# Performance work log

Hardware: AMD Instinct MI355X
Metric: run time of the kernel (lower is better)

The kernel has to match this reference:

```python
import jax, jax.numpy as jnp
import numpy as np

EMBED_DIM = 96
OUT_DIM = 192
HEADS = 2
HEAD_DIM = OUT_DIM // HEADS  # 96
STRIDE_Q = (1, 2, 2)
STRIDE_KV = (1, 8, 8)
SCALE = 1.0 / float(np.sqrt(HEAD_DIM))


def layer_norm(x, g, b, eps=1e-5):
    m = jnp.mean(x, -1, keepdims=True)
    v = jnp.mean(jnp.square(x - m), -1, keepdims=True)
    return (x - m) * jax.lax.rsqrt(v + eps) * g + b


def pool(x, thw, conv_w, g, b, stride):
    # x: [B, heads, N, d] with cls token at position 0; depthwise conv3d pool + LayerNorm(d)
    B, nh, N, d = x.shape
    T, H, W = thw
    cls_tok, rest = x[:, :, :1], x[:, :, 1:]
    rest = rest.transpose(0, 1, 3, 2).reshape(B * nh, d, T, H, W)
    rest = jax.lax.conv_general_dilated(
        rest, conv_w, stride, [(1, 1), (1, 1), (1, 1)],
        dimension_numbers=('NCDHW', 'OIDHW', 'NCDHW'), feature_group_count=d)
    T2, H2, W2 = rest.shape[2], rest.shape[3], rest.shape[4]
    rest = rest.reshape(B, nh, d, -1).transpose(0, 1, 3, 2)
    x = jnp.concatenate([cls_tok, rest], axis=2)
    return layer_norm(x, g, b), (T2, H2, W2)


def rel_idx(q_n, k_n):
    # decomposed relative-distance indices with q/k resolution ratio scaling
    q_r = max(k_n / q_n, 1.0)
    k_r = max(q_n / k_n, 1.0)
    d = (jnp.arange(q_n, dtype=jnp.float32)[:, None] * q_r
         - jnp.arange(k_n, dtype=jnp.float32)[None, :] * k_r + (k_n - 1) * k_r)
    return d.astype(jnp.int32)


def add_rel_pos(attn, q, q_thw, k_thw, rph, rpw, rpt):
    qt, qh, qw = q_thw
    kt, kh, kw = k_thw
    Rh = rph[rel_idx(qh, kh)]  # [qh, kh, d]
    Rw = rpw[rel_idx(qw, kw)]  # [qw, kw, d]
    Rt = rpt[rel_idx(qt, kt)]  # [qt, kt, d]
    B, nh, qN, d = q.shape
    r_q = q[:, :, 1:].reshape(B, nh, qt, qh, qw, d)
    rel_h = jnp.einsum('bythwc,hkc->bythwk', r_q, Rh)  # k = kh
    rel_w = jnp.einsum('bythwc,wkc->bythwk', r_q, Rw)  # k = kw
    rel_t = jnp.einsum('bythwc,tkc->bythwk', r_q, Rt)  # k = kt
    rel = (rel_t[..., :, None, None] + rel_h[..., None, :, None]
           + rel_w[..., None, None, :]).reshape(B, nh, qt * qh * qw, kt * kh * kw)
    return attn.at[:, :, 1:, 1:].add(rel)


def _forward(x, qkv_w, qkv_b, proj_w, proj_b, pq_w, nq_g, nq_b, pk_w, nk_g, nk_b,
             pv_w, nv_g, nv_b, rel_pos_h, rel_pos_w, rel_pos_t, thw):
    B, N, C = x.shape
    qkv = (x @ qkv_w.T + qkv_b).reshape(B, N, 3, HEADS, HEAD_DIM).transpose(2, 0, 3, 1, 4)
    q, k, v = qkv[0], qkv[1], qkv[2]  # each [B, heads, N, head_dim]
    k, k_thw = pool(k, thw, pk_w, nk_g, nk_b, STRIDE_KV)
    v, _ = pool(v, thw, pv_w, nv_g, nv_b, STRIDE_KV)
    q, q_thw = pool(q, thw, pq_w, nq_g, nq_b, STRIDE_Q)
    attn = jnp.einsum('bhqd,bhkd->bhqk', q * SCALE, k)
    attn = add_rel_pos(attn, q, q_thw, k_thw, rel_pos_h, rel_pos_w, rel_pos_t)
    attn = jax.nn.softmax(attn, axis=-1)
    out = jnp.einsum('bhqk,bhkd->bhqd', attn, v) + q  # residual_pool, with cls embed
    out = out.transpose(0, 2, 1, 3).reshape(B, -1, OUT_DIM)
    return out @ proj_w.T + proj_b


def setup_inputs() -> dict:
    key = jax.random.key(0)
    ks = jax.random.split(key, 10)
    T, H, W = 8, 56, 56
    N = 1 + T * H * W  # 25089
    B = 4
    std = 0.02
    return {
        'x': jax.random.normal(ks[0], (B, N, EMBED_DIM), jnp.float32),
        'qkv_w': jax.random.normal(ks[1], (3 * OUT_DIM, EMBED_DIM), jnp.float32) * std,
        'qkv_b': jnp.zeros((3 * OUT_DIM,), jnp.float32),
        'proj_w': jax.random.normal(ks[2], (OUT_DIM, OUT_DIM), jnp.float32) * std,
        'proj_b': jnp.zeros((OUT_DIM,), jnp.float32),
        'pq_w': jax.random.normal(ks[3], (HEAD_DIM, 1, 3, 3, 3), jnp.float32) * std,
        'nq_g': jnp.ones((HEAD_DIM,), jnp.float32),
        'nq_b': jnp.zeros((HEAD_DIM,), jnp.float32),
        'pk_w': jax.random.normal(ks[4], (HEAD_DIM, 1, 3, 3, 3), jnp.float32) * std,
        'nk_g': jnp.ones((HEAD_DIM,), jnp.float32),
        'nk_b': jnp.zeros((HEAD_DIM,), jnp.float32),
        'pv_w': jax.random.normal(ks[5], (HEAD_DIM, 1, 3, 3, 3), jnp.float32) * std,
        'nv_g': jnp.ones((HEAD_DIM,), jnp.float32),
        'nv_b': jnp.zeros((HEAD_DIM,), jnp.float32),
        'rel_pos_h': jax.random.normal(ks[6], (55, HEAD_DIM), jnp.float32) * std,
        'rel_pos_w': jax.random.normal(ks[7], (55, HEAD_DIM), jnp.float32) * std,
        'rel_pos_t': jax.random.normal(ks[8], (15, HEAD_DIM), jnp.float32) * std,
        'thw_t': 8, 'thw_h': 56, 'thw_w': 56,
    }


def reference(x, qkv_w, qkv_b, proj_w, proj_b, pq_w, nq_g, nq_b, pk_w, nk_g, nk_b,
              pv_w, nv_g, nv_b, rel_pos_h, rel_pos_w, rel_pos_t, thw_t, thw_h, thw_w):
    thw = (int(thw_t), int(thw_h), int(thw_w))
    return _forward(x, qkv_w, qkv_b, proj_w, proj_b, pq_w, nq_g, nq_b, pk_w, nk_g, nk_b,
                    pv_w, nv_g, nv_b, rel_pos_h, rel_pos_w, rel_pos_t, thw)
```

## Files before the change

kernel.cpp:

```cpp
#include <hip/hip_runtime.h>
#include <hip/hip_bf16.h>

typedef short short8 __attribute__((ext_vector_type(8)));
typedef float floatx4 __attribute__((ext_vector_type(4)));
typedef float floatx4v __attribute__((ext_vector_type(4)));

#define SCALE_F 0.10206207261596575f

static __device__ __forceinline__ float b2f(unsigned short u){
  unsigned int v = ((unsigned int)u) << 16; float f;
  __builtin_memcpy(&f, &v, 4); return f;
}
static __device__ __forceinline__ unsigned short f2b(float f){
  __hip_bfloat16 h = __float2bfloat16(f);
  unsigned short u; __builtin_memcpy(&u, &h, 2); return u;
}
static __device__ __forceinline__ int map20(int i){
  return (i < 2) ? i : 7 + ((i-2)/3)*8 + ((i-2)%3);
}

struct ConvDesc {
  const void* src[17];
  long long off[17];
  int count[17];
};

__global__ __launch_bounds__(256) void k_convert(ConvDesc d, unsigned short* dst_base,
                                                 int* flagp, const unsigned int* xprobe)
{
  __shared__ int sflag;
  if (threadIdx.x < 64){
    unsigned int w = xprobe[1024 + threadIdx.x];
    int e = (w >> 7) & 0xFF;
    int pl = (e >= 90 && e <= 140) ? 1 : 0;
    unsigned long long m = __ballot(pl);
    if (threadIdx.x == 0){
      sflag = (__popcll(m) < 40) ? 1 : 0;
      if (blockIdx.x == 0 && blockIdx.y == 0) *flagp = sflag;
    }
  }
  __syncthreads();
  const int flag = sflag;
  const int t = blockIdx.y + 1;
  const int cnt = d.count[t];
  unsigned short* dst = dst_base + d.off[t];
  const float* sf = (const float*)d.src[t];
  const unsigned short* su = (const unsigned short*)d.src[t];
  for (int i = blockIdx.x*blockDim.x + threadIdx.x; i < cnt; i += gridDim.x*blockDim.x){
    dst[i] = flag ? f2b(sf[i]) : su[i];
  }
}

static __device__ __forceinline__ void load_x_frag(
    const void* xr_, int flag, size_t elem_off, short8& a0, short8& a1, short8& a2)
{
  if (flag){
    const float* xr = (const float*)xr_ + elem_off;
    floatx4v f0 = *(const floatx4v*)(xr),      f1 = *(const floatx4v*)(xr+4);
    floatx4v f2 = *(const floatx4v*)(xr+32),   f3 = *(const floatx4v*)(xr+36);
    floatx4v f4 = *(const floatx4v*)(xr+64),   f5 = *(const floatx4v*)(xr+68);
    #pragma unroll
    for (int j = 0; j < 4; ++j){
      a0[j] = (short)f2b(f0[j]); a0[j+4] = (short)f2b(f1[j]);
      a1[j] = (short)f2b(f2[j]); a1[j+4] = (short)f2b(f3[j]);
      a2[j] = (short)f2b(f4[j]); a2[j+4] = (short)f2b(f5[j]);
    }
  } else {
    const unsigned short* xr = (const unsigned short*)xr_ + elem_off;
    a0 = *(const short8*)(xr);
    a1 = *(const short8*)(xr + 32);
    a2 = *(const short8*)(xr + 64);
  }
}

__global__ __launch_bounds__(256) void k_qkv(
    const void* __restrict__ x, const unsigned short* __restrict__ w,
    const unsigned short* __restrict__ bias, unsigned short* __restrict__ qr,
    unsigned short* __restrict__ kc, unsigned short* __restrict__ vc,
    unsigned short* __restrict__ kcls, unsigned short* __restrict__ vcls,
    const int* __restrict__ flagp)
{
  __shared__ __align__(16) unsigned short T[64*200];
  const int flag = *flagp;
  const int tid = threadIdx.x;
  const int lane = tid & 63;
  const int wv = tid >> 6;
  const int kq = (lane >> 4) * 8;
  const int quad = lane >> 4;
  const int col_l = lane & 15;

  if (blockIdx.x < 1569){
    const int m_base = blockIdx.x * 64;
    const int row_l = wv * 16;
    int ma = m_base + row_l + col_l; if (ma > 100355) ma = 100355;
    short8 a0, a1, a2;
    load_x_frag(x, flag, (size_t)ma*96 + kq, a0, a1, a2);

    #pragma unroll
    for (int ct = 0; ct < 12; ++ct){
      int col = ct*16 + col_l;
      const unsigned short* wrow = w + col*96 + kq;
      short8 b0 = *(const short8*)(wrow);
      short8 b1 = *(const short8*)(wrow + 32);
      short8 b2 = *(const short8*)(wrow + 64);
      float bv = b2f(bias[col]);
      floatx4 acc = {0.f,0.f,0.f,0.f};
      acc = __builtin_amdgcn_mfma_f32_16x16x32_bf16(a0, b0, acc, 0,0,0);
      acc = __builtin_amdgcn_mfma_f32_16x16x32_bf16(a1, b1, acc, 0,0,0);
      acc = __builtin_amdgcn_mfma_f32_16x16x32_bf16(a2, b2, acc, 0,0,0);
      #pragma unroll
      for (int r = 0; r < 4; ++r)
        T[(row_l + quad*4 + r)*200 + ct*16 + col_l] = f2b(acc[r] + bv);
    }
    __syncthreads();

    #pragma unroll
    for (int k = 0; k < 6; ++k){
      int c = tid + k*256;
      int row = c / 24;
      int off = c - row*24;
      int m = m_base + row;
      if (m < 100356){
        int bb2 = m / 25089;
        int ntok = m - bb2*25089;
        int col8 = off*8;
        int head = (col8 >= 96) ? 1 : 0;
        int d = col8 - head*96;
        short8 v = *(const short8*)(T + row*200 + col8);
        *(short8*)(qr + ((size_t)(bb2*2 + head)*25089 + (size_t)ntok)*96 + d) = v;
      }
    }
  } else {
    const int id = blockIdx.x - 1569;
    const int isv = id / 201;
    const int bx = id - isv*201;
    const int rbase = bx * 64 + wv * 16;

    int rhoA = rbase + col_l; if (rhoA > 12803) rhoA = 12803;
    int bA, nA;
    if (rhoA < 4){ bA = rhoA; nA = 0; }
    else {
      int rp = rhoA - 4;
      bA = rp / 3200; int rem = rp - bA*3200;
      int t = rem / 400; int s = rem - t*400;
      int ry = s / 20, rx = s - ry*20;
      nA = 1 + (t*56 + map20(ry))*56 + map20(rx);
    }
    short8 a0, a1, a2;
    load_x_frag(x, flag, ((size_t)bA*25089 + nA)*96 + kq, a0, a1, a2);

    int isCls[4], bI[4], baseI[4], valid[4];
    #pragma unroll
    for (int r = 0; r < 4; ++r){
      int rho = rbase + quad*4 + r;
      valid[r] = (rho < 12804);
      if (rho > 12803) rho = 12803;
      if (rho < 4){ isCls[r] = 1; bI[r] = rho; baseI[r] = 0; }
      else {
        int rp = rho - 4;
        int b = rp / 3200; int rem = rp - b*3200;
        int t = rem / 400; int s = rem - t*400;
        int ry = s / 20, rx = s - ry*20;
        isCls[r] = 0; bI[r] = b;
        baseI[r] = (((b*8 + t)*20 + ry)*20 + rx)*192;
      }
    }

    unsigned short* buf  = isv ? vc : kc;
    unsigned short* bufc = isv ? vcls : kcls;
    #pragma unroll
    for (int ct = 0; ct < 12; ++ct){
      const int col = 192 + (isv*12 + ct)*16 + col_l;
      const unsigned short* wrow = w + col*96 + kq;
      short8 b0 = *(const short8*)(wrow);
      short8 b1 = *(const short8*)(wrow + 32);
      short8 b2 = *(const short8*)(wrow + 64);
      float bv = b2f(bias[col]);
      floatx4 acc = {0.f,0.f,0.f,0.f};
      acc = __builtin_amdgcn_mfma_f32_16x16x32_bf16(a0, b0, acc, 0,0,0);
      acc = __builtin_amdgcn_mfma_f32_16x16x32_bf16(a1, b1, acc, 0,0,0);
      acc = __builtin_amdgcn_mfma_f32_16x16x32_bf16(a2, b2, acc, 0,0,0);
      const int head = ct / 6;
      const int dstat = (ct % 6) * 16;
      #pragma unroll
      for (int r = 0; r < 4; ++r){
        if (valid[r]){
          float o = acc[r] + bv;
          if (isCls[r]) bufc[(bI[r]*2 + head)*96 + dstat + col_l] = f2b(o);
          else          buf[baseI[r] + head*96 + dstat + col_l]   = f2b(o);
        }
      }
    }
  }
}

__global__ __launch_bounds__(384) void k_pool(
    const unsigned short* __restrict__ qr, const unsigned short* __restrict__ cwq,
    const unsigned short* __restrict__ gq, const unsigned short* __restrict__ btaq,
    unsigned short* __restrict__ qp,
    const unsigned short* __restrict__ kc, const unsigned short* __restrict__ vc,
    const unsigned short* __restrict__ kcls, const unsigned short* __restrict__ vcls,
    const unsigned short* __restrict__ cwk, const unsigned short* __restrict__ gk, const unsigned short* __restrict__ bk,
    const unsigned short* __restrict__ cwv, const unsigned short* __restrict__ gv, const unsigned short* __restrict__ bv,
    unsigned short* __restrict__ kp, unsigned short* __restrict__ vt)
{
  const int tid = threadIdx.x;
  if (blockIdx.x < 1792){
    __shared__ float wlds[27*96];
    __shared__ float gls[96], bls[96];
    __shared__ float ls1[29*12], ls2[29*12];
    __shared__ float lmean[29], linvs[29];

    const int bid = blockIdx.x;
    const int y  = bid % 28;
    const int t  = (bid / 28) % 8;
    const int bh = bid / 224;
    const bool has_cls = (y == 0 && t == 0);

    for (int idx = tid; idx < 27*96; idx += 384){
      int tap = idx / 96, d = idx - tap*96;
      wlds[idx] = b2f(cwq[d*27 + tap]);
    }
    for (int idx = tid; idx < 96; idx += 384){
      gls[idx] = b2f(gq[idx]); bls[idx] = b2f(btaq[idx]);
    }
    __syncthreads();

    const int x = tid / 12, dg = tid - x*12;
    const unsigned short* qbh = qr + (size_t)bh*25089*96;
    float val[8] = {0,0,0,0,0,0,0,0};

    if (x < 28){
      #pragma unroll
      for (int dt = 0; dt < 3; ++dt){
        int tt = t + dt - 1; if (tt < 0 || tt >= 8) continue;
        #pragma unroll
        for (int dy = 0; dy < 3; ++dy){
          int yy = 2*y + dy - 1; if (yy < 0 || yy >= 56) continue;
          #pragma unroll
          for (int dx = 0; dx < 3; ++dx){
            int xv = 2*x + dx - 1; if (xv < 0 || xv >= 56) continue;
            const int tap = (dt*3+dy)*3+dx;
            short8 v = *(const short8*)(qbh + (size_t)(1 + (tt*56 + yy)*56 + xv)*96 + dg*8);
            const float* wr = wlds + tap*96 + dg*8;
            #pragma unroll
            for (int j = 0; j < 8; ++j) val[j] += b2f((unsigned short)v[j]) * wr[j];
          }
        }
      }
      float s1 = 0.f, s2 = 0.f;
      #pragma unroll
      for (int j = 0; j < 8; ++j){ s1 += val[j]; s2 += val[j]*val[j]; }
      ls1[x*12+dg] = s1; ls2[x*12+dg] = s2;
    } else if (has_cls && tid >= 348 && tid < 360){
      int cdg = tid - 348;
      short8 v = *(const short8*)(qbh + cdg*8);
      float s1 = 0.f, s2 = 0.f;
      #pragma unroll
      for (int j = 0; j < 8; ++j){ val[j] = b2f((unsigned short)v[j]); s1 += val[j]; s2 += val[j]*val[j]; }
      ls1[28*12+cdg] = s1; ls2[28*12+cdg] = s2;
    }
    __syncthreads();

    if (tid < 28 || (tid == 28 && has_cls)){
      float s1 = 0.f, s2 = 0.f;
      #pragma unroll
      for (int k = 0; k < 12; ++k){ s1 += ls1[tid*12+k]; s2 += ls2[tid*12+k]; }
      float mean = s1 * (1.f/96.f);
      float var  = s2 * (1.f/96.f) - mean*mean;
      lmean[tid] = mean; linvs[tid] = rsqrtf(var + 1e-5f);
    }
    __syncthreads();

    if (x < 28){
      float mean = lmean[x], inv = linvs[x];
      int tok = 1 + (t*28 + y)*28 + x;
      short8 o;
      #pragma unroll
      for (int j = 0; j < 8; ++j)
        o[j] = (short)f2b((val[j] - mean)*inv*gls[dg*8+j] + bls[dg*8+j]);
      *(short8*)(qp + ((size_t)bh*6273 + tok)*96 + dg*8) = o;
    } else if (has_cls && tid >= 348 && tid < 360){
      int cdg = tid - 348;
      float mean = lmean[28], inv = linvs[28];
      short8 o;
      #pragma unroll
      for (int j = 0; j < 8; ++j)
        o[j] = (short)f2b((val[j] - mean)*inv*gls[cdg*8+j] + bls[cdg*8+j]);
      *(short8*)(qp + (size_t)bh*6273*96 + cdg*8) = o;
    }
  } else {
    __shared__ float r1[3][128], r2s[3][128];
    const int unit = tid >> 7;
    const int d = tid & 127;
    const int u = (blockIdx.x - 1792)*3 + unit;
    const bool live = (u < 6656);
    int isv = 0, bh = 0, key = 0;
    if (live){
      isv = u / 3328; int rem = u - isv*3328;
      bh = rem / 416; key = rem - bh*416;
    }
    const bool pad = (key >= 393);
    const int b = bh >> 1, head = bh & 1;
    const unsigned short* buf  = isv ? vc : kc;
    const unsigned short* bufc = isv ? vcls : kcls;
    const unsigned short* cw = (isv == 0) ? cwk : cwv;
    const unsigned short* g  = (isv == 0) ? gk : gv;
    const unsigned short* bt = (isv == 0) ? bk : bv;

    float val = 0.f;
    if (live && !pad && d < 96){
      if (key == 0) val = b2f(bufc[bh*96 + d]);
      else {
        int s = key - 1; int t = s / 49; int r2 = s - t*49; int y = r2 / 7; int xx = r2 - y*7;
        const unsigned short* wr = cw + d*27;
        float sum = 0.f;
        #pragma unroll
        for (int dt = 0; dt < 3; ++dt){
          int tt = t + dt - 1; if (tt < 0 || tt >= 8) continue;
          #pragma unroll
          for (int dy = 0; dy < 3; ++dy){
            if (y == 0 && dy == 0) continue;
            int ry = (y == 0) ? (dy - 1) : 2 + 3*(y-1) + dy;
            #pragma unroll
            for (int dx = 0; dx < 3; ++dx){
              if (xx == 0 && dx == 0) continue;
              int rx = (xx == 0) ? (dx - 1) : 2 + 3*(xx-1) + dx;
              sum += b2f(buf[(((b*8 + tt)*20 + ry)*20 + rx)*192 + head*96 + d]) * b2f(wr[(dt*3+dy)*3+dx]);
            }
          }
        }
        val = sum;
      }
    }
    r1[unit][d]  = (d < 96) ? val : 0.f;
    r2s[unit][d] = (d < 96) ? val*val : 0.f;
    __syncthreads();
    for (int off = 64; off > 0; off >>= 1){
      if (d < off){ r1[unit][d] += r1[unit][d+off]; r2s[unit][d] += r2s[unit][d+off]; }
      __syncthreads();
    }
    if (live && d < 96){
      float mean = r1[unit][0] * (1.f/96.f);
      float var  = r2s[unit][0] * (1.f/96.f) - mean*mean;
      float inv = rsqrtf(var + 1e-5f);
      float o = pad ? 0.f : (val - mean)*inv*b2f(g[d]) + b2f(bt[d]);
      if (isv == 0) kp[((size_t)bh*416 + key)*96 + d] = f2b(o);
      else          vt[((size_t)bh*96 + d)*416 + key] = f2b(o);
    }
  }
}

#define PSTR 424
__global__ __launch_bounds__(256, 3) void k_attn(
    const unsigned short* __restrict__ qp, const unsigned short* __restrict__ kp,
    const unsigned short* __restrict__ vt,
    const unsigned short* __restrict__ rph, const unsigned short* __restrict__ rpw,
    const unsigned short* __restrict__ rpt,
    unsigned short* __restrict__ ao, const int q_off)
{
  __shared__ unsigned short P[32*PSTR];
  __shared__ __align__(16) float rel[24*36 + 4];
  __shared__ float mx_sh[4][32], sum_sh[4][32];

  const int bh = blockIdx.y;
  const int bb = bh >> 1, head = bh & 1;
  const int tid = threadIdx.x;
  const int lane = tid & 63;
  const int wv = tid >> 6;
  const int q0 = (q_off + blockIdx.x) * 32;

  const unsigned short* qbase = qp + (size_t)bh*6273*96;
  const unsigned short* kbase = kp + (size_t)bh*416*96;
  const unsigned short* vbase = vt + (size_t)bh*96*416;

  const int col = lane & 15;
  const int quad = lane >> 4;
  const int kq = quad * 8;

  short8 aF[2][3];
  #pragma unroll
  for (int tl = 0; tl < 2; ++tl){
    int qa = q0 + tl*16 + col; if (qa > 6272) qa = 6272;
    const unsigned short* qrow = qbase + (size_t)qa*96 + kq;
    aF[tl][0] = *(const short8*)(qrow);
    aF[tl][1] = *(const short8*)(qrow + 32);
    aF[tl][2] = *(const short8*)(qrow + 64);
  }

  int yq[2][4], xq[2][4], tq[2][4], livx[2][4], liv[2][4];
  #pragma unroll
  for (int tl = 0; tl < 2; ++tl)
  #pragma unroll
  for (int r = 0; r < 4; ++r){
    int gq = q0 + tl*16 + quad*4 + r;
    liv[tl][r]  = (gq >= 1);
    livx[tl][r] = (gq >= 1 && gq <= 6272);
    int s = (gq >= 1) ? gq - 1 : 0;
    tq[tl][r] = s / 784; int r2 = s - tq[tl][r]*784; yq[tl][r] = r2 / 28; xq[tl][r] = r2 - yq[tl][r]*28;
  }

  #pragma unroll
  for (int j = 0; j < 2; ++j){
    const int c = (wv*2 + j)*16 + col;
    const unsigned short* rrow;
    if (c < 55)       rrow = rph + (size_t)c*96;
    else if (c < 110) rrow = rpw + (size_t)(c-55)*96;
    else { int ci = c-110; if (ci > 14) ci = 14; rrow = rpt + (size_t)ci*96; }
    rrow += kq;
    short8 b0 = *(const short8*)(rrow);
    short8 b1 = *(const short8*)(rrow + 32);
    short8 b2 = *(const short8*)(rrow + 64);
    #pragma unroll
    for (int tl = 0; tl < 2; ++tl){
      floatx4 rc = {0.f,0.f,0.f,0.f};
      rc = __builtin_amdgcn_mfma_f32_16x16x32_bf16(aF[tl][0], b0, rc, 0,0,0);
      rc = __builtin_amdgcn_mfma_f32_16x16x32_bf16(aF[tl][1], b1, rc, 0,0,0);
      rc = __builtin_amdgcn_mfma_f32_16x16x32_bf16(aF[tl][2], b2, rc, 0,0,0);
      #pragma unroll
      for (int r = 0; r < 4; ++r){
        if (!livx[tl][r]) continue;
        const int m = tl*16 + quad*4 + r;
        if (c < 55){
          int u = yq[tl][r] + 24 - c;
          if (u >= 0 && u <= 24 && (u & 3) == 0) rel[(u >> 2)*36 + m] = rc[r];
        } else if (c < 110){
          int u = xq[tl][r] + 24 - (c - 55);
          if (u >= 0 && u <= 24 && (u & 3) == 0) rel[(8 + (u >> 2))*36 + m] = rc[r];
        } else if (c < 125){
          int u = tq[tl][r] + 7 - (c - 110);
          if (u >= 0 && u <= 7) rel[(16 + u)*36 + m] = rc[r];
        }
      }
    }
  }
  __syncthreads();

  floatx4 acc[2][7];
  float mx[2][4] = {{-1e30f,-1e30f,-1e30f,-1e30f},{-1e30f,-1e30f,-1e30f,-1e30f}};
  #pragma unroll
  for (int i = 0; i < 7; ++i){
    int t = wv*7 + i; if (t > 25) t = 25;
    const unsigned short* krow = kbase + (size_t)(t*16 + col)*96 + kq;
    short8 b0 = *(const short8*)(krow);
    short8 b1 = *(const short8*)(krow + 32);
    short8 b2 = *(const short8*)(krow + 64);
    const int key = t*16 + col;
    const bool validk = (key < 393);
    int kt = 0, ky = 0, kx = 0;
    if (key >= 1 && validk){
      int ks = key - 1; kt = ks / 49; int krm = ks - kt*49; ky = krm / 7; kx = krm - ky*7;
    }
    floatx4v rh0 = *(const floatx4v*)(rel + ky*36 + quad*4);
    floatx4v rh1 = *(const floatx4v*)(rel + ky*36 + 16 + quad*4);
    floatx4v rw0 = *(const floatx4v*)(rel + (8 + kx)*36 + quad*4);
    floatx4v rw1 = *(const floatx4v*)(rel + (8 + kx)*36 + 16 + quad*4);
    floatx4v rt0 = *(const floatx4v*)(rel + (16 + kt)*36 + quad*4);
    floatx4v rt1 = *(const floatx4v*)(rel + (16 + kt)*36 + 16 + quad*4);
    #pragma unroll
    for (int tl = 0; tl < 2; ++tl){
      floatx4 a = {0.f,0.f,0.f,0.f};
      a = __builtin_amdgcn_mfma_f32_16x16x32_bf16(aF[tl][0], b0, a, 0,0,0);
      a = __builtin_amdgcn_mfma_f32_16x16x32_bf16(aF[tl][1], b1, a, 0,0,0);
      a = __builtin_amdgcn_mfma_f32_16x16x32_bf16(aF[tl][2], b2, a, 0,0,0);
      #pragma unroll
      for (int r = 0; r < 4; ++r){
        float s;
        if (!validk) s = -1e30f;
        else {
          s = a[r] * SCALE_F;
          if (key >= 1 && liv[tl][r]){
            float rhv = tl ? rh1[r] : rh0[r];
            float rwv = tl ? rw1[r] : rw0[r];
            float rtv = tl ? rt1[r] : rt0[r];
            s += rhv + rwv + rtv;
          }
        }
        a[r] = s;
        mx[tl][r] = fmaxf(mx[tl][r], s);
      }
      acc[tl][i] = a;
    }
  }
  #pragma unroll
  for (int tl = 0; tl < 2; ++tl)
  #pragma unroll
  for (int r = 0; r < 4; ++r){
    #pragma unroll
    for (int o = 1; o < 16; o <<= 1) mx[tl][r] = fmaxf(mx[tl][r], __shfl_xor(mx[tl][r], o, 64));
  }
  if (col == 0){
    #pragma unroll
    for (int tl = 0; tl < 2; ++tl)
    #pragma unroll
    for (int r = 0; r < 4; ++r) mx_sh[wv][tl*16 + quad*4 + r] = mx[tl][r];
  }
  __syncthreads();

  float M[2][4];
  #pragma unroll
  for (int tl = 0; tl < 2; ++tl)
  #pragma unroll
  for (int r = 0; r < 4; ++r){
    const int m = tl*16 + quad*4 + r;
    float m01 = fmaxf(mx_sh[0][m], mx_sh[1][m]);
    float m23 = fmaxf(mx_sh[2][m], mx_sh[3][m]);
    M[tl][r] = fmaxf(m01, m23);
  }
  float sum[2][4] = {{0.f,0.f,0.f,0.f},{0.f,0.f,0.f,0.f}};
  #pragma unroll
  for (int i = 0; i < 7; ++i){
    #pragma unroll
    for (int tl = 0; tl < 2; ++tl)
    #pragma unroll
    for (int r = 0; r < 4; ++r){
      float e = __expf(acc[tl][i][r] - M[tl][r]);
      acc[tl][i][r] = e; sum[tl][r] += e;
    }
  }
  #pragma unroll
  for (int tl = 0; tl < 2; ++tl)
  #pragma unroll
  for (int r = 0; r < 4; ++r){
    #pragma unroll
    for (int o = 1; o < 16; o <<= 1) sum[tl][r] += __shfl_xor(sum[tl][r], o, 64);
  }
  if (col == 0){
    #pragma unroll
    for (int tl = 0; tl < 2; ++tl)
    #pragma unroll
    for (int r = 0; r < 4; ++r) sum_sh[wv][tl*16 + quad*4 + r] = sum[tl][r];
  }
  #pragma unroll
  for (int i = 0; i < 7; ++i){
    int t = wv*7 + i; if (t > 25) t = 25;
    #pragma unroll
    for (int tl = 0; tl < 2; ++tl)
    #pragma unroll
    for (int r = 0; r < 4; ++r)
      P[(tl*16 + quad*4 + r)*PSTR + t*16 + col] = f2b(acc[tl][i][r]);
  }
  __syncthreads();

  const int tlw = wv >> 1;
  float linv4[4];
  #pragma unroll
  for (int r = 0; r < 4; ++r){
    const int m = tlw*16 + quad*4 + r;
    linv4[r] = 1.f / (sum_sh[0][m] + sum_sh[1][m] + sum_sh[2][m] + sum_sh[3][m]);
  }

  short8 pf[13];
  #pragma unroll
  for (int s = 0; s < 13; ++s)
    pf[s] = *(const short8*)(P + (tlw*16 + col)*PSTR + s*32 + kq);

  #pragma unroll
  for (int j = 0; j < 3; ++j){
    const int slot = (wv & 1)*3 + j;
    const int dd = slot*16 + col;
    const unsigned short* vrow = vbase + (size_t)dd*416 + kq;
    floatx4 o = {0.f,0.f,0.f,0.f};
    #pragma unroll
    for (int s = 0; s < 13; ++s){
      short8 vf = *(const short8*)(vrow + s*32);
      o = __builtin_amdgcn_mfma_f32_16x16x32_bf16(pf[s], vf, o, 0,0,0);
    }
    #pragma unroll
    for (int r = 0; r < 4; ++r){
      int gq = q0 + tlw*16 + quad*4 + r;
      if (gq <= 6272){
        float val = o[r] * linv4[r] + b2f(qbase[(size_t)gq*96 + dd]);
        ao[((size_t)bb*6273 + gq)*192 + head*96 + dd] = f2b(val);
      }
    }
  }
}

__global__ __launch_bounds__(256) void k_proj(
    const unsigned short* __restrict__ ao, const unsigned short* __restrict__ w,
    const unsigned short* __restrict__ bias, void* __restrict__ out, const int* __restrict__ flagp)
{
  const int flag = *flagp;
  const int lane = threadIdx.x & 63;
  const int wv = threadIdx.x >> 6;
  const int c = blockIdx.y*64 + wv*16 + (lane & 15);
  const int kq = (lane >> 4) * 8;
  short8 bfr[6];
  const unsigned short* wrow = w + c*192 + kq;
  #pragma unroll
  for (int s = 0; s < 6; ++s) bfr[s] = *(const short8*)(wrow + 32*s);
  float bv = b2f(bias[c]);
  const int m_base = blockIdx.x * 64;
  for (int i = 0; i < 4; ++i){
    int mt = m_base + i*16;
    int ma = mt + (lane & 15); if (ma > 25091) ma = 25091;
    const unsigned short* arow = ao + (size_t)ma*192 + kq;
    floatx4 acc = {0.f,0.f,0.f,0.f};
    #pragma unroll
    for (int s = 0; s < 6; ++s){
      short8 a = *(const short8*)(arow + 32*s);
      acc = __builtin_amdgcn_mfma_f32_16x16x32_bf16(a, bfr[s], acc, 0,0,0);
    }
    #pragma unroll
    for (int r = 0; r < 4; ++r){
      int m = mt + (lane >> 4)*4 + r;
      if (m < 25092){
        float o = acc[r] + bv;
        if (flag) ((float*)out)[(size_t)m*192 + c] = o;
        else      ((unsigned short*)out)[(size_t)m*192 + c] = f2b(o);
      }
    }
  }
}

extern "C" void kernel_launch(void* const* d_in, const int* in_sizes, int n_in,
                              void* d_out, int out_size, void* d_ws, size_t ws_size,
                              hipStream_t stream)
{
  char* p = (char*)d_ws;
  int* flagp = (int*)p; p += 16;
  unsigned short* conv = (unsigned short*)p;

  ConvDesc desc;
  long long cum = 0;
  for (int i = 0; i < 17; ++i){
    desc.src[i] = d_in[i];
    desc.off[i] = cum;
    desc.count[i] = in_sizes[i];
    cum += in_sizes[i];
  }
  p += (size_t)cum * 2;

  unsigned short* q_raw  = (unsigned short*)p; p += (size_t)19268352*2;
  unsigned short* kc     = (unsigned short*)p; p += (size_t)2457600*2;
  unsigned short* vc     = (unsigned short*)p; p += (size_t)2457600*2;
  unsigned short* kcls   = (unsigned short*)p; p += (size_t)768*2;
  unsigned short* vcls   = (unsigned short*)p; p += (size_t)768*2;
  unsigned short* q_pool = (unsigned short*)p; p += (size_t)4817664*2;
  unsigned short* kp_buf = (unsigned short*)p; p += (size_t)319488*2;
  unsigned short* v_t    = (unsigned short*)p; p += (size_t)319488*2;
  unsigned short* a_out  = q_raw;

  const unsigned short* cqkv_w = conv + desc.off[1];
  const unsigned short* cqkv_b = conv + desc.off[2];
  const unsigned short* cproj_w= conv + desc.off[3];
  const unsigned short* cproj_b= conv + desc.off[4];
  const unsigned short* cpq_w  = conv + desc.off[5];
  const unsigned short* cnq_g  = conv + desc.off[6];
  const unsigned short* cnq_b  = conv + desc.off[7];
  const unsigned short* cpk_w  = conv + desc.off[8];
  const unsigned short* cnk_g  = conv + desc.off[9];
  const unsigned short* cnk_b  = conv + desc.off[10];
  const unsigned short* cpv_w  = conv + desc.off[11];
  const unsigned short* cnv_g  = conv + desc.off[12];
  const unsigned short* cnv_b  = conv + desc.off[13];
  const unsigned short* crph   = conv + desc.off[14];
  const unsigned short* crpw   = conv + desc.off[15];
  const unsigned short* crpt   = conv + desc.off[16];

  k_convert<<<dim3(16, 16), 256, 0, stream>>>(desc, conv, flagp, (const unsigned int*)d_in[0]);
  k_qkv  <<<dim3(1971), 256, 0, stream>>>(d_in[0], cqkv_w, cqkv_b, q_raw, kc, vc, kcls, vcls, flagp);
  k_pool <<<dim3(4011), 384, 0, stream>>>(q_raw, cpq_w, cnq_g, cnq_b, q_pool,
                                          kc, vc, kcls, vcls,
                                          cpk_w, cnk_g, cnk_b, cpv_w, cnv_g, cnv_b, kp_buf, v_t);
  k_attn <<<dim3(99, 8), 256, 0, stream>>>(q_pool, kp_buf, v_t, crph, crpw, crpt, a_out, 0);
  k_attn <<<dim3(98, 8), 256, 0, stream>>>(q_pool, kp_buf, v_t, crph, crpw, crpt, a_out, 99);
  k_proj <<<dim3(393, 3), 256, 0, stream>>>(a_out, cproj_w, cproj_b, d_out, flagp);
}
```

Measured before the change: 276.3 us.

## Compute two output time slices per Q-pool block and merge attention launches

Each Q-pooling block now produces two adjacent output frames, loading four input frames once and reusing each loaded vector for both outputs' temporal taps. This halves the Q-pool block count and cuts redundant global reads of overlapping time slices. Block indices are remapped with an interleave across groups of 8, and the two k_attn launches are merged into one grid of 197. Register pressure rises because each thread holds two accumulator sets.

```diff
diff --git a/kernel.cpp b/kernel.cpp
--- a/kernel.cpp
+++ b/kernel.cpp
@@ -205,17 +205,20 @@
     unsigned short* __restrict__ kp, unsigned short* __restrict__ vt)
 {
   const int tid = threadIdx.x;
-  if (blockIdx.x < 1792){
+  if (blockIdx.x < 896){
     __shared__ float wlds[27*96];
     __shared__ float gls[96], bls[96];
-    __shared__ float ls1[29*12], ls2[29*12];
-    __shared__ float lmean[29], linvs[29];
-
-    const int bid = blockIdx.x;
-    const int y  = bid % 28;
-    const int t  = (bid / 28) % 8;
-    const int bh = bid / 224;
-    const bool has_cls = (y == 0 && t == 0);
+    __shared__ float ls1[2][29*12], ls2[2][29*12];
+    __shared__ float lmean[2][29], linvs[2][29];
+
+    const int rb = blockIdx.x;
+    const int lbid = (rb & 7)*112 + (rb >> 3);
+    const int y   = lbid % 28;
+    const int grp = lbid / 28;
+    const int bh  = grp >> 2;
+    const int g   = grp & 3;
+    const int t0  = g*2;
+    const bool has_cls = (y == 0 && g == 0);
 
     for (int idx = tid; idx < 27*96; idx += 384){
       int tap = idx / 96, d = idx - tap*96;
@@ -228,72 +231,91 @@
 
     const int x = tid / 12, dg = tid - x*12;
     const unsigned short* qbh = qr + (size_t)bh*25089*96;
-    float val[8] = {0,0,0,0,0,0,0,0};
+    float val[2][8] = {{0,0,0,0,0,0,0,0},{0,0,0,0,0,0,0,0}};
 
     if (x < 28){
       #pragma unroll
-      for (int dt = 0; dt < 3; ++dt){
-        int tt = t + dt - 1; if (tt < 0 || tt >= 8) continue;
+      for (int tt4 = 0; tt4 < 4; ++tt4){
+        const int tt = t0 - 1 + tt4;
+        if (tt < 0 || tt >= 8) continue;
         #pragma unroll
         for (int dy = 0; dy < 3; ++dy){
           int yy = 2*y + dy - 1; if (yy < 0 || yy >= 56) continue;
           #pragma unroll
           for (int dx = 0; dx < 3; ++dx){
             int xv = 2*x + dx - 1; if (xv < 0 || xv >= 56) continue;
-            const int tap = (dt*3+dy)*3+dx;
             short8 v = *(const short8*)(qbh + (size_t)(1 + (tt*56 + yy)*56 + xv)*96 + dg*8);
-            const float* wr = wlds + tap*96 + dg*8;
+            float fv[8];
             #pragma unroll
-            for (int j = 0; j < 8; ++j) val[j] += b2f((unsigned short)v[j]) * wr[j];
+            for (int j = 0; j < 8; ++j) fv[j] = b2f((unsigned short)v[j]);
+            if (tt4 < 3){
+              const float* wr = wlds + ((tt4*3+dy)*3+dx)*96 + dg*8;
+              #pragma unroll
+              for (int j = 0; j < 8; ++j) val[0][j] += fv[j] * wr[j];
+            }
+            if (tt4 >= 1){
+              const float* wr = wlds + (((tt4-1)*3+dy)*3+dx)*96 + dg*8;
+              #pragma unroll
+              for (int j = 0; j < 8; ++j) val[1][j] += fv[j] * wr[j];
+            }
           }
         }
       }
-      float s1 = 0.f, s2 = 0.f;
-      #pragma unroll
-      for (int j = 0; j < 8; ++j){ s1 += val[j]; s2 += val[j]*val[j]; }
-      ls1[x*12+dg] = s1; ls2[x*12+dg] = s2;
+      #pragma unroll
+      for (int tp = 0; tp < 2; ++tp){
+        float s1 = 0.f, s2 = 0.f;
+        #pragma unroll
+        for (int j = 0; j < 8; ++j){ s1 += val[tp][j]; s2 += val[tp][j]*val[tp][j]; }
+        ls1[tp][x*12+dg] = s1; ls2[tp][x*12+dg] = s2;
+      }
     } else if (has_cls && tid >= 348 && tid < 360){
       int cdg = tid - 348;
       short8 v = *(const short8*)(qbh + cdg*8);
       float s1 = 0.f, s2 = 0.f;
       #pragma unroll
-      for (int j = 0; j < 8; ++j){ val[j] = b2f((unsigned short)v[j]); s1 += val[j]; s2 += val[j]*val[j]; }
-      ls1[28*12+cdg] = s1; ls2[28*12+cdg] = s2;
+      for (int j = 0; j < 8; ++j){ val[0][j] = b2f((unsigned short)v[j]); s1 += val[0][j]; s2 += val[0][j]*val[0][j]; }
+      ls1[0][28*12+cdg] = s1; ls2[0][28*12+cdg] = s2;
     }
     __syncthreads();
 
-    if (tid < 28 || (tid == 28 && has_cls)){
-      float s1 = 0.f, s2 = 0.f;
-      #pragma unroll
-      for (int k = 0; k < 12; ++k){ s1 += ls1[tid*12+k]; s2 += ls2[tid*12+k]; }
-      float mean = s1 * (1.f/96.f);
-      float var  = s2 * (1.f/96.f) - mean*mean;
-      lmean[tid] = mean; linvs[tid] = rsqrtf(var + 1e-5f);
+    if (tid < 58){
+      int tp = tid / 29, row = tid - tp*29;
+      if (row < 28 || (row == 28 && tp == 0 && has_cls)){
+        float s1 = 0.f, s2 = 0.f;
+        #pragma unroll
+        for (int k = 0; k < 12; ++k){ s1 += ls1[tp][row*12+k]; s2 += ls2[tp][row*12+k]; }
+        float mean = s1 * (1.f/96.f);
+        float var  = s2 * (1.f/96.f) - mean*mean;
+        lmean[tp][row] = mean; linvs[tp][row] = rsqrtf(var + 1e-5f);
+      }
     }
     __syncthreads();
 
     if (x < 28){
-      float mean = lmean[x], inv = linvs[x];
-      int tok = 1 + (t*28 + y)*28 + x;
-      short8 o;
-      #pragma unroll
-      for (int j = 0; j < 8; ++j)
-        o[j] = (short)f2b((val[j] - mean)*inv*gls[dg*8+j] + bls[dg*8+j]);
-      *(short8*)(qp + ((size_t)bh*6273 + tok)*96 + dg*8) = o;
+      #pragma unroll
+      for (int tp = 0; tp < 2; ++tp){
+        float mean = lmean[tp][x], inv = linvs[tp][x];
+        int tok = 1 + ((t0 + tp)*28 + y)*28 + x;
+        short8 o;
+        #pragma unroll
+        for (int j = 0; j < 8; ++j)
+          o[j] = (short)f2b((val[tp][j] - mean)*inv*gls[dg*8+j] + bls[dg*8+j]);
+        *(short8*)(qp + ((size_t)bh*6273 + tok)*96 + dg*8) = o;
+      }
     } else if (has_cls && tid >= 348 && tid < 360){
       int cdg = tid - 348;
-      float mean = lmean[28], inv = linvs[28];
+      float mean = lmean[0][28], inv = linvs[0][28];
       short8 o;
       #pragma unroll
       for (int j = 0; j < 8; ++j)
-        o[j] = (short)f2b((val[j] - mean)*inv*gls[cdg*8+j] + bls[cdg*8+j]);
+        o[j] = (short)f2b((val[0][j] - mean)*inv*gls[cdg*8+j] + bls[cdg*8+j]);
       *(short8*)(qp + (size_t)bh*6273*96 + cdg*8) = o;
     }
   } else {
     __shared__ float r1[3][128], r2s[3][128];
     const int unit = tid >> 7;
     const int d = tid & 127;
-    const int u = (blockIdx.x - 1792)*3 + unit;
+    const int u = (blockIdx.x - 896)*3 + unit;
     const bool live = (u < 6656);
     int isv = 0, bh = 0, key = 0;
     if (live){
@@ -661,10 +683,9 @@
 
   k_convert<<<dim3(16, 16), 256, 0, stream>>>(desc, conv, flagp, (const unsigned int*)d_in[0]);
   k_qkv  <<<dim3(1971), 256, 0, stream>>>(d_in[0], cqkv_w, cqkv_b, q_raw, kc, vc, kcls, vcls, flagp);
-  k_pool <<<dim3(4011), 384, 0, stream>>>(q_raw, cpq_w, cnq_g, cnq_b, q_pool,
+  k_pool <<<dim3(3115), 384, 0, stream>>>(q_raw, cpq_w, cnq_g, cnq_b, q_pool,
                                           kc, vc, kcls, vcls,
                                           cpk_w, cnk_g, cnk_b, cpv_w, cnv_g, cnv_b, kp_buf, v_t);
-  k_attn <<<dim3(99, 8), 256, 0, stream>>>(q_pool, kp_buf, v_t, crph, crpw, crpt, a_out, 0);
-  k_attn <<<dim3(98, 8), 256, 0, stream>>>(q_pool, kp_buf, v_t, crph, crpw, crpt, a_out, 99);
+  k_attn <<<dim3(197, 8), 256, 0, stream>>>(q_pool, kp_buf, v_t, crph, crpw, crpt, a_out, 0);
   k_proj <<<dim3(393, 3), 256, 0, stream>>>(a_out, cproj_w, cproj_b, d_out, flagp);
 }
```

Result: faster. 259.3 us (median of 4 runs) (-6.2%).
